# Kernel optimization log

Hardware: AMD Instinct MI355X
Metric: run time of the kernel (lower is better)

## Reference

```python
import jax, jax.numpy as jnp
import numpy as np

NEG_BIG = -9e15

def setup_inputs() -> dict:
    key = jax.random.key(0)
    k1, k2, k3, k4, k5 = jax.random.split(key, 5)
    B, N, Fin, Fout = 32768, 15, 128, 128
    x = jax.random.normal(k1, (B, N, Fin), dtype=jnp.float32)
    adj = jax.random.randint(k2, (B, N, N), 0, 2, dtype=jnp.int32)
    W = jax.random.normal(k3, (Fin, Fout), dtype=jnp.float32) * (1.414 / np.sqrt(Fin))
    a_src = jax.random.normal(k4, (Fout,), dtype=jnp.float32) * 0.1
    a_dst = jax.random.normal(k5, (Fout,), dtype=jnp.float32) * 0.1
    return {"x": x, "adj": adj, "W": W, "a_src": a_src, "a_dst": a_dst}

def reference(x, adj, W, a_src, a_dst):
    alpha = 0.2  # leaky relu negative slope
    h = jnp.einsum('bnf,fo->bno', x, W)            # [B,N,Fout]
    s_src = jnp.einsum('bno,o->bn', h, a_src)      # contribution of node i
    s_dst = jnp.einsum('bno,o->bn', h, a_dst)      # contribution of node j
    # e[b,i,j] = leakyrelu(a . concat(h_i, h_j))
    e = jax.nn.leaky_relu(s_src[:, :, None] + s_dst[:, None, :], negative_slope=alpha)
    att = jnp.where(adj > 0, e, NEG_BIG)
    # NOTE: original applies softmax over dim=1 (the i axis), faithfully reproduced
    att = jax.nn.softmax(att, axis=1)
    # dropout skipped (eval mode)
    h_prime = jax.nn.elu(jnp.einsum('bij,bjo->bio', att, h))
    return h_prime
```

## Files before the change

### kernel.cpp

```cpp
#include <hip/hip_runtime.h>
#include <hip/hip_bf16.h>

typedef __attribute__((ext_vector_type(4))) float f32x4;
typedef __attribute__((ext_vector_type(8))) short short8;
typedef __attribute__((ext_vector_type(4))) _Float16 f16x4;

__device__ __forceinline__ short f2bf(float f) {
    unsigned u = __builtin_bit_cast(unsigned, f);
    u += 0x7fffu + ((u >> 16) & 1u);
    return (short)(unsigned short)(u >> 16);
}

__global__ void gat_pre(const float* __restrict__ W, const float* __restrict__ a_src,
                        const float* __restrict__ a_dst, unsigned short* __restrict__ wt,
                        float* __restrict__ wa) {
    int blk = blockIdx.x, t = threadIdx.x;
    if (blk < 8) {
        int e = blk * 256 + t;
        int kk = e >> 9, ct = (e >> 6) & 7, lane = e & 63;
        int lq = lane >> 4, l15 = lane & 15;
        short8 v;
#pragma unroll
        for (int jj = 0; jj < 8; ++jj)
            v[jj] = f2bf(W[(kk * 32 + lq * 8 + jj) * 128 + ct * 16 + l15]);
        *(short8*)(wt + (size_t)e * 8) = v;
    } else if (t < 128) {
        float s1 = 0.f, s2 = 0.f;
        for (int o = 0; o < 128; ++o) {
            float w = W[t * 128 + o];
            s1 += w * a_src[o];
            s2 += w * a_dst[o];
        }
        wa[t] = s1; wa[128 + t] = s2;
    }
}

__device__ __forceinline__ void load_batch(const float* __restrict__ x,
                                           const int* __restrict__ adj,
                                           int b, int lq, int l15,
                                           float4 (&xv)[8], int (&av)[4]) {
    const float* xb = x + (size_t)b * 1920 + l15 * 128 + lq * 8;
#pragma unroll
    for (int kk = 0; kk < 4; ++kk) {
        if (l15 < 15) {
            xv[2 * kk]     = *(const float4*)(xb + kk * 32);
            xv[2 * kk + 1] = *(const float4*)(xb + kk * 32 + 4);
        } else {
            xv[2 * kk]     = make_float4(0.f, 0.f, 0.f, 0.f);
            xv[2 * kk + 1] = make_float4(0.f, 0.f, 0.f, 0.f);
        }
    }
    const int* ab = adj + (size_t)b * 225 + l15 * 15 + lq * 4;
#pragma unroll
    for (int r = 0; r < 4; ++r)
        av[r] = (l15 < 15 && lq * 4 + r < 15) ? ab[r] : 0;
}

__device__ __forceinline__ void prep(const float4 (&xv)[8], const float* __restrict__ walds,
                                     int lq, float& ps, float& pd, short8 (&af)[4]) {
    ps = 0.f; pd = 0.f;
#pragma unroll
    for (int kk = 0; kk < 4; ++kk) {
        float4 a0 = xv[2 * kk], a1 = xv[2 * kk + 1];
        const float* wb = walds + kk * 32 + lq * 8;
        float4 s0 = *(const float4*)(wb);
        float4 s1 = *(const float4*)(wb + 4);
        float4 d0 = *(const float4*)(wb + 128);
        float4 d1 = *(const float4*)(wb + 132);
        ps += a0.x * s0.x + a0.y * s0.y + a0.z * s0.z + a0.w * s0.w
            + a1.x * s1.x + a1.y * s1.y + a1.z * s1.z + a1.w * s1.w;
        pd += a0.x * d0.x + a0.y * d0.y + a0.z * d0.z + a0.w * d0.w
            + a1.x * d1.x + a1.y * d1.y + a1.z * d1.z + a1.w * d1.w;
        short8 c;
        c[0] = f2bf(a0.x); c[1] = f2bf(a0.y); c[2] = f2bf(a0.z); c[3] = f2bf(a0.w);
        c[4] = f2bf(a1.x); c[5] = f2bf(a1.y); c[6] = f2bf(a1.z); c[7] = f2bf(a1.w);
        af[kk] = c;
    }
}

__global__ __launch_bounds__(256, 3) void gat_main(
    const float* __restrict__ x, const int* __restrict__ adj,
    const unsigned short* __restrict__ wfrag, const float* __restrict__ wa,
    float* __restrict__ out, int B)
{
    __shared__ __align__(16) unsigned short wlds[16384];
    __shared__ __align__(16) float walds[256];
    __shared__ __align__(16) float stg[4 * 8 * 132];

    const int t = threadIdx.x;
    const int wv = t >> 6;
    const int lane = t & 63;
    const int lq = lane >> 4, l15 = lane & 15;

#pragma unroll
    for (int i = 0; i < 8; ++i)
        *(float4*)((char*)wlds + (t + 256 * i) * 16) =
            *(const float4*)((const char*)wfrag + (t + 256 * i) * 16);
    if (t < 64)
        *(float4*)(walds + t * 4) = *(const float4*)(wa + t * 4);
    __syncthreads();

    const int wid = blockIdx.x * 4 + wv;
    const int stride = gridDim.x * 4;

    float4 xr[8];
    int adjr[4];
    short8 af[4];
    float ps = 0.f, pd = 0.f;
    int adjc[4] = {0, 0, 0, 0};

    if (wid < B) {
        load_batch(x, adj, wid, lq, l15, xr, adjr);
        prep(xr, walds, lq, ps, pd, af);
#pragma unroll
        for (int r = 0; r < 4; ++r) adjc[r] = adjr[r];
    }

    float* const wbuf = &stg[wv * 8 * 132];
    const int fswW = ((l15 & 1) << 2) | (l15 & 2);

    for (int b = wid; b < B; b += stride) {
        const int bn = b + stride;
        const bool pn = bn < B;
        if (pn) load_batch(x, adj, bn, lq, l15, xr, adjr);
        __builtin_amdgcn_sched_barrier(0);

        float ss = ps + __shfl_xor(ps, 16);
        ss += __shfl_xor(ss, 32);
        float sd = pd + __shfl_xor(pd, 16);
        sd += __shfl_xor(sd, 32);

        f32x4 acc[8];
#pragma unroll
        for (int ct = 0; ct < 8; ++ct) acc[ct] = (f32x4){0.f, 0.f, 0.f, 0.f};
#pragma unroll
        for (int kk = 0; kk < 4; ++kk) {
#pragma unroll
            for (int ct = 0; ct < 8; ++ct) {
                short8 bf = *(const short8*)(wlds + ((size_t)(kk * 8 + ct) * 64 + lane) * 8);
                acc[ct] = __builtin_amdgcn_mfma_f32_16x16x32_bf16(af[kk], bf, acc[ct], 0, 0, 0);
            }
        }

        float attv[4];
#pragma unroll
        for (int r = 0; r < 4; ++r) {
            float sdj = __shfl(sd, lq * 4 + r);
            float e = ss + sdj;
            e = e > 0.f ? e : 0.2f * e;
            e = fminf(e, 30.f);
            float pexp = adjc[r] > 0 ? __expf(e) : 1e-26f;
            if (l15 == 15) pexp = 0.f;
            float sm = pexp;
            sm += __shfl_xor(sm, 1);
            sm += __shfl_xor(sm, 2);
            sm += __shfl_xor(sm, 4);
            sm += __shfl_xor(sm, 8);
            attv[r] = pexp * __builtin_amdgcn_rcpf(sm);
        }

        f16x4 attf;
        attf[0] = (_Float16)attv[0]; attf[1] = (_Float16)attv[1];
        attf[2] = (_Float16)attv[2]; attf[3] = (_Float16)attv[3];

        const f32x4 z4 = {0.f, 0.f, 0.f, 0.f};
        f32x4 dq[8];
#pragma unroll
        for (int ct = 0; ct < 8; ++ct) {
            f16x4 hA;
            hA[0] = (_Float16)acc[ct][0]; hA[1] = (_Float16)acc[ct][1];
            hA[2] = (_Float16)acc[ct][2]; hA[3] = (_Float16)acc[ct][3];
            f32x4 o4 = __builtin_amdgcn_mfma_f32_16x16x16f16(hA, attf, z4, 0, 0, 0);
#pragma unroll
            for (int r = 0; r < 4; ++r) {
                float u = o4[r];
                o4[r] = u > 0.f ? u : (__expf(u) - 1.f);
            }
            dq[ct] = o4;
        }

        float* const obase = out + (size_t)b * 1920;
#pragma unroll
        for (int p = 0; p < 2; ++p) {
            if ((l15 >> 3) == p) {
#pragma unroll
                for (int ct = 0; ct < 8; ++ct) {
                    int qs = (ct * 4 + lq) ^ fswW;
                    *(f32x4*)(wbuf + (l15 & 7) * 132 + qs * 4) = dq[ct];
                }
            }
            asm volatile("s_waitcnt lgkmcnt(0)" ::: "memory");
#pragma unroll
            for (int it = 0; it < 4; ++it) {
                int Q = p * 256 + it * 64 + lane;
                if (Q < 480) {
                    int orr = Q >> 5;
                    int qs = (Q & 31) ^ (((orr & 1) << 2) | (orr & 2));
                    f32x4 val = *(const f32x4*)(wbuf + (orr & 7) * 132 + qs * 4);
                    *(f32x4*)(obase + (size_t)Q * 4) = val;
                }
            }
            asm volatile("" ::: "memory");
        }

        if (pn) {
            prep(xr, walds, lq, ps, pd, af);
#pragma unroll
            for (int r = 0; r < 4; ++r) adjc[r] = adjr[r];
        }
    }
}

extern "C" void kernel_launch(void* const* d_in, const int* in_sizes, int n_in,
                              void* d_out, int out_size, void* d_ws, size_t ws_size,
                              hipStream_t stream) {
    const float* x     = (const float*)d_in[0];
    const int*   adj   = (const int*)d_in[1];
    const float* W     = (const float*)d_in[2];
    const float* a_src = (const float*)d_in[3];
    const float* a_dst = (const float*)d_in[4];
    float* out = (float*)d_out;

    unsigned short* wt = (unsigned short*)d_ws;
    float* wa = (float*)((char*)d_ws + 32768);

    int B = in_sizes[0] / (15 * 128);

    gat_pre<<<9, 256, 0, stream>>>(W, a_src, a_dst, wt, wa);
    gat_main<<<1024, 256, 0, stream>>>(x, adj, wt, wa, out, B);
}
```

Baseline: 117.2 us.

## Replace persistent prefetching loop with one-batch-per-wave grid launch

Drops the persistent grid-stride loop, which ran 1024 blocks and prefetched the next batch's x and adj into registers. The kernel now launches one wave per batch element (B/4 blocks), and each wave issues its global x/adj loads before staging W fragments into LDS so the two overlap. This relies on many resident waves to hide memory latency instead of software prefetch, at the cost of re-staging the 32 KB W fragment per block. There is no bounds check on b, so correctness assumes B is a multiple of 4.

```diff
diff --git a/kernel.cpp b/kernel.cpp
--- a/kernel.cpp
+++ b/kernel.cpp
@@ -35,33 +35,55 @@
     }
 }
 
-__device__ __forceinline__ void load_batch(const float* __restrict__ x,
-                                           const int* __restrict__ adj,
-                                           int b, int lq, int l15,
-                                           float4 (&xv)[8], int (&av)[4]) {
-    const float* xb = x + (size_t)b * 1920 + l15 * 128 + lq * 8;
+__global__ __launch_bounds__(256, 3) void gat_main(
+    const float* __restrict__ x, const int* __restrict__ adj,
+    const unsigned short* __restrict__ wfrag, const float* __restrict__ wa,
+    float* __restrict__ out, int B)
+{
+    __shared__ __align__(16) unsigned short wlds[16384];
+    __shared__ __align__(16) float walds[256];
+    __shared__ __align__(16) float stg[4 * 8 * 132];
+
+    const int t = threadIdx.x;
+    const int wv = t >> 6;
+    const int lane = t & 63;
+    const int lq = lane >> 4, l15 = lane & 15;
+
+    const int b = blockIdx.x * 4 + wv;
+
+    float4 xr[8];
+    int adjr[4];
+    {
+        const float* xb = x + (size_t)b * 1920 + l15 * 128 + lq * 8;
+#pragma unroll
+        for (int kk = 0; kk < 4; ++kk) {
+            if (l15 < 15) {
+                xr[2 * kk]     = *(const float4*)(xb + kk * 32);
+                xr[2 * kk + 1] = *(const float4*)(xb + kk * 32 + 4);
+            } else {
+                xr[2 * kk]     = make_float4(0.f, 0.f, 0.f, 0.f);
+                xr[2 * kk + 1] = make_float4(0.f, 0.f, 0.f, 0.f);
+            }
+        }
+        const int* ab = adj + (size_t)b * 225 + l15 * 15 + lq * 4;
+#pragma unroll
+        for (int r = 0; r < 4; ++r)
+            adjr[r] = (l15 < 15 && lq * 4 + r < 15) ? ab[r] : 0;
+    }
+
+#pragma unroll
+    for (int i = 0; i < 8; ++i)
+        *(float4*)((char*)wlds + (t + 256 * i) * 16) =
+            *(const float4*)((const char*)wfrag + (t + 256 * i) * 16);
+    if (t < 64)
+        *(float4*)(walds + t * 4) = *(const float4*)(wa + t * 4);
+    __syncthreads();
+
+    float ps = 0.f, pd = 0.f;
+    short8 af[4];
 #pragma unroll
     for (int kk = 0; kk < 4; ++kk) {
-        if (l15 < 15) {
-            xv[2 * kk]     = *(const float4*)(xb + kk * 32);
-            xv[2 * kk + 1] = *(const float4*)(xb + kk * 32 + 4);
-        } else {
-            xv[2 * kk]     = make_float4(0.f, 0.f, 0.f, 0.f);
-            xv[2 * kk + 1] = make_float4(0.f, 0.f, 0.f, 0.f);
-        }
-    }
-    const int* ab = adj + (size_t)b * 225 + l15 * 15 + lq * 4;
-#pragma unroll
-    for (int r = 0; r < 4; ++r)
-        av[r] = (l15 < 15 && lq * 4 + r < 15) ? ab[r] : 0;
-}
-
-__device__ __forceinline__ void prep(const float4 (&xv)[8], const float* __restrict__ walds,
-                                     int lq, float& ps, float& pd, short8 (&af)[4]) {
-    ps = 0.f; pd = 0.f;
-#pragma unroll
-    for (int kk = 0; kk < 4; ++kk) {
-        float4 a0 = xv[2 * kk], a1 = xv[2 * kk + 1];
+        float4 a0 = xr[2 * kk], a1 = xr[2 * kk + 1];
         const float* wb = walds + kk * 32 + lq * 8;
         float4 s0 = *(const float4*)(wb);
         float4 s1 = *(const float4*)(wb + 4);
@@ -76,138 +98,85 @@
         c[4] = f2bf(a1.x); c[5] = f2bf(a1.y); c[6] = f2bf(a1.z); c[7] = f2bf(a1.w);
         af[kk] = c;
     }
-}
-
-__global__ __launch_bounds__(256, 3) void gat_main(
-    const float* __restrict__ x, const int* __restrict__ adj,
-    const unsigned short* __restrict__ wfrag, const float* __restrict__ wa,
-    float* __restrict__ out, int B)
-{
-    __shared__ __align__(16) unsigned short wlds[16384];
-    __shared__ __align__(16) float walds[256];
-    __shared__ __align__(16) float stg[4 * 8 * 132];
-
-    const int t = threadIdx.x;
-    const int wv = t >> 6;
-    const int lane = t & 63;
-    const int lq = lane >> 4, l15 = lane & 15;
-
-#pragma unroll
-    for (int i = 0; i < 8; ++i)
-        *(float4*)((char*)wlds + (t + 256 * i) * 16) =
-            *(const float4*)((const char*)wfrag + (t + 256 * i) * 16);
-    if (t < 64)
-        *(float4*)(walds + t * 4) = *(const float4*)(wa + t * 4);
-    __syncthreads();
-
-    const int wid = blockIdx.x * 4 + wv;
-    const int stride = gridDim.x * 4;
-
-    float4 xr[8];
-    int adjr[4];
-    short8 af[4];
-    float ps = 0.f, pd = 0.f;
-    int adjc[4] = {0, 0, 0, 0};
-
-    if (wid < B) {
-        load_batch(x, adj, wid, lq, l15, xr, adjr);
-        prep(xr, walds, lq, ps, pd, af);
-#pragma unroll
-        for (int r = 0; r < 4; ++r) adjc[r] = adjr[r];
+
+    float ss = ps + __shfl_xor(ps, 16);
+    ss += __shfl_xor(ss, 32);
+    float sd = pd + __shfl_xor(pd, 16);
+    sd += __shfl_xor(sd, 32);
+
+    f32x4 acc[8];
+#pragma unroll
+    for (int ct = 0; ct < 8; ++ct) acc[ct] = (f32x4){0.f, 0.f, 0.f, 0.f};
+#pragma unroll
+    for (int kk = 0; kk < 4; ++kk) {
+#pragma unroll
+        for (int ct = 0; ct < 8; ++ct) {
+            short8 bf = *(const short8*)(wlds + ((size_t)(kk * 8 + ct) * 64 + lane) * 8);
+            acc[ct] = __builtin_amdgcn_mfma_f32_16x16x32_bf16(af[kk], bf, acc[ct], 0, 0, 0);
+        }
+    }
+
+    float attv[4];
+#pragma unroll
+    for (int r = 0; r < 4; ++r) {
+        float sdj = __shfl(sd, lq * 4 + r);
+        float e = ss + sdj;
+        e = e > 0.f ? e : 0.2f * e;
+        e = fminf(e, 30.f);
+        float pexp = adjr[r] > 0 ? __expf(e) : 1e-26f;
+        if (l15 == 15) pexp = 0.f;
+        float sm = pexp;
+        sm += __shfl_xor(sm, 1);
+        sm += __shfl_xor(sm, 2);
+        sm += __shfl_xor(sm, 4);
+        sm += __shfl_xor(sm, 8);
+        attv[r] = pexp * __builtin_amdgcn_rcpf(sm);
+    }
+
+    f16x4 attf;
+    attf[0] = (_Float16)attv[0]; attf[1] = (_Float16)attv[1];
+    attf[2] = (_Float16)attv[2]; attf[3] = (_Float16)attv[3];
+
+    const f32x4 z4 = {0.f, 0.f, 0.f, 0.f};
+    f32x4 dq[8];
+#pragma unroll
+    for (int ct = 0; ct < 8; ++ct) {
+        f16x4 hA;
+        hA[0] = (_Float16)acc[ct][0]; hA[1] = (_Float16)acc[ct][1];
+        hA[2] = (_Float16)acc[ct][2]; hA[3] = (_Float16)acc[ct][3];
+        f32x4 o4 = __builtin_amdgcn_mfma_f32_16x16x16f16(hA, attf, z4, 0, 0, 0);
+#pragma unroll
+        for (int r = 0; r < 4; ++r) {
+            float u = o4[r];
+            o4[r] = u > 0.f ? u : (__expf(u) - 1.f);
+        }
+        dq[ct] = o4;
     }
 
     float* const wbuf = &stg[wv * 8 * 132];
     const int fswW = ((l15 & 1) << 2) | (l15 & 2);
-
-    for (int b = wid; b < B; b += stride) {
-        const int bn = b + stride;
-        const bool pn = bn < B;
-        if (pn) load_batch(x, adj, bn, lq, l15, xr, adjr);
-        __builtin_amdgcn_sched_barrier(0);
-
-        float ss = ps + __shfl_xor(ps, 16);
-        ss += __shfl_xor(ss, 32);
-        float sd = pd + __shfl_xor(pd, 16);
-        sd += __shfl_xor(sd, 32);
-
-        f32x4 acc[8];
-#pragma unroll
-        for (int ct = 0; ct < 8; ++ct) acc[ct] = (f32x4){0.f, 0.f, 0.f, 0.f};
-#pragma unroll
-        for (int kk = 0; kk < 4; ++kk) {
+    float* const obase = out + (size_t)b * 1920;
+#pragma unroll
+    for (int p = 0; p < 2; ++p) {
+        if ((l15 >> 3) == p) {
 #pragma unroll
             for (int ct = 0; ct < 8; ++ct) {
-                short8 bf = *(const short8*)(wlds + ((size_t)(kk * 8 + ct) * 64 + lane) * 8);
-                acc[ct] = __builtin_amdgcn_mfma_f32_16x16x32_bf16(af[kk], bf, acc[ct], 0, 0, 0);
+                int qs = (ct * 4 + lq) ^ fswW;
+                *(f32x4*)(wbuf + (l15 & 7) * 132 + qs * 4) = dq[ct];
             }
         }
-
-        float attv[4];
-#pragma unroll
-        for (int r = 0; r < 4; ++r) {
-            float sdj = __shfl(sd, lq * 4 + r);
-            float e = ss + sdj;
-            e = e > 0.f ? e : 0.2f * e;
-            e = fminf(e, 30.f);
-            float pexp = adjc[r] > 0 ? __expf(e) : 1e-26f;
-            if (l15 == 15) pexp = 0.f;
-            float sm = pexp;
-            sm += __shfl_xor(sm, 1);
-            sm += __shfl_xor(sm, 2);
-            sm += __shfl_xor(sm, 4);
-            sm += __shfl_xor(sm, 8);
-            attv[r] = pexp * __builtin_amdgcn_rcpf(sm);
-        }
-
-        f16x4 attf;
-        attf[0] = (_Float16)attv[0]; attf[1] = (_Float16)attv[1];
-        attf[2] = (_Float16)attv[2]; attf[3] = (_Float16)attv[3];
-
-        const f32x4 z4 = {0.f, 0.f, 0.f, 0.f};
-        f32x4 dq[8];
-#pragma unroll
-        for (int ct = 0; ct < 8; ++ct) {
-            f16x4 hA;
-            hA[0] = (_Float16)acc[ct][0]; hA[1] = (_Float16)acc[ct][1];
-            hA[2] = (_Float16)acc[ct][2]; hA[3] = (_Float16)acc[ct][3];
-            f32x4 o4 = __builtin_amdgcn_mfma_f32_16x16x16f16(hA, attf, z4, 0, 0, 0);
-#pragma unroll
-            for (int r = 0; r < 4; ++r) {
-                float u = o4[r];
-                o4[r] = u > 0.f ? u : (__expf(u) - 1.f);
+        asm volatile("s_waitcnt lgkmcnt(0)" ::: "memory");
+#pragma unroll
+        for (int it = 0; it < 4; ++it) {
+            int Q = p * 256 + it * 64 + lane;
+            if (Q < 480) {
+                int orr = Q >> 5;
+                int qs = (Q & 31) ^ (((orr & 1) << 2) | (orr & 2));
+                f32x4 val = *(const f32x4*)(wbuf + (orr & 7) * 132 + qs * 4);
+                *(f32x4*)(obase + (size_t)Q * 4) = val;
             }
-            dq[ct] = o4;
-        }
-
-        float* const obase = out + (size_t)b * 1920;
-#pragma unroll
-        for (int p = 0; p < 2; ++p) {
-            if ((l15 >> 3) == p) {
-#pragma unroll
-                for (int ct = 0; ct < 8; ++ct) {
-                    int qs = (ct * 4 + lq) ^ fswW;
-                    *(f32x4*)(wbuf + (l15 & 7) * 132 + qs * 4) = dq[ct];
-                }
-            }
-            asm volatile("s_waitcnt lgkmcnt(0)" ::: "memory");
-#pragma unroll
-            for (int it = 0; it < 4; ++it) {
-                int Q = p * 256 + it * 64 + lane;
-                if (Q < 480) {
-                    int orr = Q >> 5;
-                    int qs = (Q & 31) ^ (((orr & 1) << 2) | (orr & 2));
-                    f32x4 val = *(const f32x4*)(wbuf + (orr & 7) * 132 + qs * 4);
-                    *(f32x4*)(obase + (size_t)Q * 4) = val;
-                }
-            }
-            asm volatile("" ::: "memory");
-        }
-
-        if (pn) {
-            prep(xr, walds, lq, ps, pd, af);
-#pragma unroll
-            for (int r = 0; r < 4; ++r) adjc[r] = adjr[r];
-        }
+        }
+        asm volatile("" ::: "memory");
     }
 }
 
@@ -225,7 +194,8 @@
     float* wa = (float*)((char*)d_ws + 32768);
 
     int B = in_sizes[0] / (15 * 128);
+    int nblk = (B + 3) / 4;
 
     gat_pre<<<9, 256, 0, stream>>>(W, a_src, a_dst, wt, wa);
-    gat_main<<<1024, 256, 0, stream>>>(x, adj, wt, wa, out, B);
-}
+    gat_main<<<nblk, 256, 0, stream>>>(x, adj, wt, wa, out, B);
+}
```

Result: slower. 148.9 us (+27.1%).
